# Performance work log

Measured on AMD Instinct MI355X. Metric: run time of the kernel, lower is better.

## Reference

```python
import jax, jax.numpy as jnp
import numpy as np

N_EMB = 100000
REPR = 512
BATCH = 8192
HIST = 50
DROP_P = 0.2  # fraction of positions set to -1 sentinel


def setup_inputs() -> dict:
    key = jax.random.key(0)
    k_idx, k_drop, k_w = jax.random.split(key, 3)
    target = jax.random.randint(k_idx, (BATCH, HIST), 0, N_EMB, dtype=jnp.int64)
    drop = jax.random.uniform(k_drop, (BATCH, HIST)) < DROP_P
    drop = drop.at[:, 0].set(False)  # guarantee >=1 valid token per row
    target = jnp.where(drop, jnp.int64(-1), target)
    emb_weight = jax.random.normal(k_w, (N_EMB, REPR), dtype=jnp.float32)
    return {"target": target, "emb_weight": emb_weight}


def reference(target, emb_weight):
    # mask of valid (non -1) positions: [B, L]
    mask = (target != -1)
    safe_idx = jnp.where(mask, target, 0)
    # gather: [B, L, D], zero out sentinel rows, sum over L
    gathered = emb_weight[safe_idx] * mask[..., None].astype(emb_weight.dtype)
    pooled = gathered.sum(axis=1)  # [B, D]
    # original returns [B, 1, D] (each per-token emb is [1, D])
    return pooled[:, None, :]
```

## Files before the change

kernel.cpp:

```cpp
#include <hip/hip_runtime.h>

#define BATCH 8192
#define HIST  50
#define REPR  512
#define CH    10

__global__ __launch_bounds__(256) void embbag_sum_kernel(
    const int* __restrict__ target,
    const float* __restrict__ emb,
    float* __restrict__ out)
{
    const int row  = blockIdx.x * 2 + (threadIdx.x >> 7);
    const int lane = threadIdx.x & 127;

    const int* t = target + row * HIST;
    const float* col = emb + (size_t)lane * 4;

    float4 acc = make_float4(0.f, 0.f, 0.f, 0.f);

    for (int j0 = 0; j0 < HIST; j0 += CH) {
        int   idx[CH];
        float w[CH];
        float4 v[CH];

#pragma unroll
        for (int k = 0; k < CH; ++k) {
            const int ix = t[j0 + k];
            w[k]   = (ix >= 0) ? 1.0f : 0.0f;
            idx[k] = (ix >= 0) ? ix : 0;
        }

#pragma unroll
        for (int k = 0; k < CH; ++k) {
            v[k] = *reinterpret_cast<const float4*>(col + (size_t)idx[k] * REPR);
        }

#pragma unroll
        for (int k = 0; k < CH; ++k) {
            acc.x = fmaf(v[k].x, w[k], acc.x);
            acc.y = fmaf(v[k].y, w[k], acc.y);
            acc.z = fmaf(v[k].z, w[k], acc.z);
            acc.w = fmaf(v[k].w, w[k], acc.w);
        }
    }

    *reinterpret_cast<float4*>(out + (size_t)row * REPR + (size_t)lane * 4) = acc;
}

extern "C" void kernel_launch(void* const* d_in, const int* in_sizes, int n_in,
                              void* d_out, int out_size, void* d_ws, size_t ws_size,
                              hipStream_t stream) {
    const int*   target = (const int*)d_in[0];
    const float* emb    = (const float*)d_in[1];
    float*       out    = (float*)d_out;

    dim3 grid(BATCH / 2);
    dim3 block(256);
    embbag_sum_kernel<<<grid, block, 0, stream>>>(target, emb, out);
}
```

Baseline: 99.57 us.

## Bucket row indices by table slice in shared memory and skip sentinels

Each row's valid indices are compacted into shared-memory buckets by table slice using atomics, then gathered slice by slice. This drops sentinel loads and aims to improve locality of the gathers. The output is written with a nontemporal store. The cost is added syncs, atomics, and partially filled chunks per slice that issue masked dummy loads.

```diff
diff --git a/kernel.cpp b/kernel.cpp
--- a/kernel.cpp
+++ b/kernel.cpp
@@ -1,50 +1,72 @@
 #include <hip/hip_runtime.h>
 
-#define BATCH 8192
-#define HIST  50
-#define REPR  512
-#define CH    10
+#define BATCH  8192
+#define HIST   50
+#define REPR   512
+#define N_EMB  100000
+#define NSLICE 8
+#define SLICE_SZ ((N_EMB + NSLICE - 1) / NSLICE)
+#define CH     8
 
-__global__ __launch_bounds__(256) void embbag_sum_kernel(
+typedef float v4f __attribute__((ext_vector_type(4)));
+
+__global__ __launch_bounds__(256) void embbag_sliced_kernel(
     const int* __restrict__ target,
     const float* __restrict__ emb,
     float* __restrict__ out)
 {
-    const int row  = blockIdx.x * 2 + (threadIdx.x >> 7);
+    __shared__ int s_idx[2][NSLICE][HIST];
+    __shared__ int s_cnt[2][NSLICE];
+
+    const int g    = threadIdx.x >> 7;
     const int lane = threadIdx.x & 127;
+    const int row  = blockIdx.x * 2 + g;
 
-    const int* t = target + row * HIST;
+    if (lane < NSLICE) s_cnt[g][lane] = 0;
+    __syncthreads();
+    if (lane < HIST) {
+        const int ix = target[row * HIST + lane];
+        if (ix >= 0) {
+            const int b   = ix / SLICE_SZ;
+            const int pos = atomicAdd(&s_cnt[g][b], 1);
+            s_idx[g][b][pos] = ix;
+        }
+    }
+    __syncthreads();
+
     const float* col = emb + (size_t)lane * 4;
-
     float4 acc = make_float4(0.f, 0.f, 0.f, 0.f);
 
-    for (int j0 = 0; j0 < HIST; j0 += CH) {
-        int   idx[CH];
-        float w[CH];
-        float4 v[CH];
-
+    for (int p = 0; p < NSLICE; ++p) {
+        const int n = s_cnt[g][p];
+        for (int k0 = 0; k0 < n; k0 += CH) {
+            int    idx[CH];
+            float  w[CH];
+            float4 v[CH];
 #pragma unroll
-        for (int k = 0; k < CH; ++k) {
-            const int ix = t[j0 + k];
-            w[k]   = (ix >= 0) ? 1.0f : 0.0f;
-            idx[k] = (ix >= 0) ? ix : 0;
-        }
-
+            for (int k = 0; k < CH; ++k) {
+                const bool valid = (k0 + k) < n;
+                idx[k] = valid ? s_idx[g][p][k0 + k] : 0;
+                w[k]   = valid ? 1.0f : 0.0f;
+            }
 #pragma unroll
-        for (int k = 0; k < CH; ++k) {
-            v[k] = *reinterpret_cast<const float4*>(col + (size_t)idx[k] * REPR);
-        }
-
+            for (int k = 0; k < CH; ++k) {
+                v[k] = *reinterpret_cast<const float4*>(col + (size_t)idx[k] * REPR);
+            }
 #pragma unroll
-        for (int k = 0; k < CH; ++k) {
-            acc.x = fmaf(v[k].x, w[k], acc.x);
-            acc.y = fmaf(v[k].y, w[k], acc.y);
-            acc.z = fmaf(v[k].z, w[k], acc.z);
-            acc.w = fmaf(v[k].w, w[k], acc.w);
+            for (int k = 0; k < CH; ++k) {
+                acc.x = fmaf(v[k].x, w[k], acc.x);
+                acc.y = fmaf(v[k].y, w[k], acc.y);
+                acc.z = fmaf(v[k].z, w[k], acc.z);
+                acc.w = fmaf(v[k].w, w[k], acc.w);
+            }
         }
     }
 
-    *reinterpret_cast<float4*>(out + (size_t)row * REPR + (size_t)lane * 4) = acc;
+    v4f av;
+    av.x = acc.x; av.y = acc.y; av.z = acc.z; av.w = acc.w;
+    v4f* o = reinterpret_cast<v4f*>(out + (size_t)row * REPR + (size_t)lane * 4);
+    __builtin_nontemporal_store(av, o);
 }
 
 extern "C" void kernel_launch(void* const* d_in, const int* in_sizes, int n_in,
@@ -56,5 +78,5 @@
 
     dim3 grid(BATCH / 2);
     dim3 block(256);
-    embbag_sum_kernel<<<grid, block, 0, stream>>>(target, emb, out);
+    embbag_sliced_kernel<<<grid, block, 0, stream>>>(target, emb, out);
 }
```

Result: no change. 100.1 us (+0.5%).
